# Kernel optimization log

Hardware: AMD Instinct MI355X
Metric: run time of the kernel (lower is better)

## Reference

```python
import jax, jax.numpy as jnp
import numpy as np

D_MODEL = 1024
HEADS = 16
D_K = D_MODEL // HEADS


def setup_inputs() -> dict:
    key = jax.random.key(0)
    ks = jax.random.split(key, 12)
    B, S = 2, 2048
    s = 1.0 / np.sqrt(D_MODEL)
    return {
        "queries": jax.random.normal(ks[0], (B, S, D_MODEL), jnp.float32),
        "keys": jax.random.normal(ks[1], (B, S, D_MODEL), jnp.float32),
        "values": jax.random.normal(ks[2], (B, S, D_MODEL), jnp.float32),
        "Wq": jax.random.normal(ks[3], (D_MODEL, D_MODEL), jnp.float32) * s,
        "bq": jnp.zeros((D_MODEL,), jnp.float32),
        "Wk": jax.random.normal(ks[4], (D_MODEL, D_MODEL), jnp.float32) * s,
        "bk": jnp.zeros((D_MODEL,), jnp.float32),
        "Wv": jax.random.normal(ks[5], (D_MODEL, D_MODEL), jnp.float32) * s,
        "bv": jnp.zeros((D_MODEL,), jnp.float32),
        "Wo": jax.random.normal(ks[6], (D_MODEL, D_MODEL), jnp.float32) * s,
        "bo": jnp.zeros((D_MODEL,), jnp.float32),
        "gamma": jnp.ones((D_MODEL,), jnp.float32),
        "beta": jnp.zeros((D_MODEL,), jnp.float32),
    }


def reference(queries, keys, values, Wq, bq, Wk, bk, Wv, bv, Wo, bo, gamma, beta):
    B, Nq, D = queries.shape
    Nk = keys.shape[1]
    # projections (torch Linear: x @ W.T + b), split into heads
    q = (queries @ Wq.T + bq).reshape(B, Nq, HEADS, D_K).transpose(0, 2, 1, 3)  # [B,H,Nq,dk]
    k = (keys @ Wk.T + bk).reshape(B, Nk, HEADS, D_K).transpose(0, 2, 1, 3)     # [B,H,Nk,dk]
    v = (values @ Wv.T + bv).reshape(B, Nk, HEADS, D_K).transpose(0, 2, 1, 3)   # [B,H,Nk,dv]
    att = jnp.einsum("bhqd,bhkd->bhqk", q, k) / np.sqrt(D_K).astype(np.float32)
    att = jax.nn.softmax(att, axis=-1)
    out = jnp.einsum("bhqk,bhkd->bhqd", att, v)
    out = out.transpose(0, 2, 1, 3).reshape(B, Nq, HEADS * D_K)
    out = out @ Wo.T + bo
    # dropout_prob=0 -> identity; residual shortcut then LayerNorm
    out = queries + out
    mean = jnp.mean(out, axis=-1, keepdims=True)
    var = jnp.var(out, axis=-1, keepdims=True)
    out = (out - mean) / jnp.sqrt(var + 1e-5) * gamma + beta
    return out
```

## Files before the change

kernel.cpp:

```cpp
#include <hip/hip_runtime.h>

#define S_LEN 2048
#define BATCH 2
#define DM 1024
#define NH 16
#define DK 64
#define M_ROWS 4096

typedef __bf16 bf16x8 __attribute__((ext_vector_type(8)));
typedef float f32x4 __attribute__((ext_vector_type(4)));
typedef unsigned int u32;
typedef unsigned short u16;

__device__ __forceinline__ float bf2f(u16 u) {
    union { u32 i; float f; } v;
    v.i = ((u32)u) << 16;
    return v.f;
}

__device__ __forceinline__ u16 rne16(float f) {
    u32 i = __builtin_bit_cast(u32, f);
    return (u16)((i + 0x7fffu + ((i >> 16) & 1u)) >> 16);
}

__device__ __forceinline__ u32 pk2(float x, float y) {
    u32 a = __builtin_bit_cast(u32, x) + 0x8000u;
    u32 b = __builtin_bit_cast(u32, y) + 0x8000u;
    return (a >> 16) | (b & 0xffff0000u);
}

__device__ __forceinline__ void async16(const void* g, void* l) {
    __builtin_amdgcn_global_load_lds(
        (const __attribute__((address_space(1))) u32*)((unsigned long long)g),
        (__attribute__((address_space(3))) u32*)((u32)(unsigned long long)l),
        16, 0, 0);
}

__global__ __launch_bounds__(256) void cvt_all(
    const float* __restrict__ q, const float* __restrict__ k,
    const float* __restrict__ v, const float* __restrict__ wq,
    const float* __restrict__ wk, const float* __restrict__ wv,
    const float* __restrict__ wo,
    u16* q16, u16* k16, u16* v16, u16* wq16, u16* wk16, u16* wv16, u16* wo16)
{
    const int b = blockIdx.x;
    const float* src; u16* dst; long off;
    if (b < 2048)      { src = q;  dst = q16;  off = (long)b * 2048; }
    else if (b < 4096) { src = k;  dst = k16;  off = (long)(b - 2048) * 2048; }
    else if (b < 6144) { src = v;  dst = v16;  off = (long)(b - 4096) * 2048; }
    else if (b < 6656) { src = wq; dst = wq16; off = (long)(b - 6144) * 2048; }
    else if (b < 7168) { src = wk; dst = wk16; off = (long)(b - 6656) * 2048; }
    else if (b < 7680) { src = wv; dst = wv16; off = (long)(b - 7168) * 2048; }
    else               { src = wo; dst = wo16; off = (long)(b - 7680) * 2048; }
    const long i = off + (long)threadIdx.x * 8;
    const float4 a = *(const float4*)(src + i);
    const float4 c = *(const float4*)(src + i + 4);
    uint4 r;
    r.x = pk2(a.x, a.y); r.y = pk2(a.z, a.w);
    r.z = pk2(c.x, c.y); r.w = pk2(c.z, c.w);
    *(uint4*)(dst + i) = r;
}

__global__ __launch_bounds__(256) void gemm64(
    const u16* __restrict__ A0, const u16* __restrict__ W0,
    const float* __restrict__ bias0, u16* __restrict__ C0, float sc0, int md0,
    const u16* __restrict__ A1, const u16* __restrict__ W1,
    const float* __restrict__ bias1, u16* __restrict__ C1, float sc1, int md1)
{
    __shared__ u16 sA[128 * 32];
    __shared__ u16 sB[64 * 32];

    const u16* A = blockIdx.z ? A1 : A0;
    const u16* W = blockIdx.z ? W1 : W0;
    const float* bias = blockIdx.z ? bias1 : bias0;
    u16* C = blockIdx.z ? C1 : C0;
    const float scale = blockIdx.z ? sc1 : sc0;
    const int mode = blockIdx.z ? md1 : md0;

    const int t    = threadIdx.x;
    const int lane = t & 63;
    const int wave = t >> 6;
    const int quad = lane >> 4;
    const int lr   = lane & 15;
    const int wm   = wave * 32;
    const int m0   = blockIdx.y * 128;
    const int n0   = blockIdx.x * 64;

    f32x4 acc[2][4];
#pragma unroll
    for (int i = 0; i < 2; i++)
#pragma unroll
        for (int j = 0; j < 4; j++) acc[i][j] = (f32x4){0.f, 0.f, 0.f, 0.f};

    const int la1 = t + 256;
    const int ra0 = t >> 2,   ca0 = (t & 3)   ^ (ra0 & 3);
    const int ra1 = la1 >> 2, ca1 = (la1 & 3) ^ (ra1 & 3);
    const int rb  = t >> 2,   cb  = (t & 3)   ^ (rb & 3);
    const u16* gA0 = A + (long)(m0 + ra0) * 1024 + ca0 * 8;
    const u16* gA1 = A + (long)(m0 + ra1) * 1024 + ca1 * 8;
    const u16* gW  = W + (long)(n0 + rb) * 1024 + cb * 8;

    const int sw = quad ^ (lr & 3);

    for (int k0 = 0; k0 < 1024; k0 += 32) {
        __syncthreads();
        async16(gA0 + k0, &sA[t * 8]);
        async16(gA1 + k0, &sA[la1 * 8]);
        async16(gW + k0, &sB[t * 8]);
        __syncthreads();

        bf16x8 aF[2], bF[4];
#pragma unroll
        for (int i = 0; i < 2; i++)
            aF[i] = *(const bf16x8*)&sA[((wm + i * 16 + lr) * 4 + sw) * 8];
#pragma unroll
        for (int j = 0; j < 4; j++)
            bF[j] = *(const bf16x8*)&sB[((j * 16 + lr) * 4 + sw) * 8];
#pragma unroll
        for (int i = 0; i < 2; i++)
#pragma unroll
            for (int j = 0; j < 4; j++)
                acc[i][j] = __builtin_amdgcn_mfma_f32_16x16x32_bf16(
                    aF[i], bF[j], acc[i][j], 0, 0, 0);
    }

#pragma unroll
    for (int j = 0; j < 4; j++) {
        const int gn = n0 + j * 16 + lr;
        const float bvv = bias[gn];
#pragma unroll
        for (int i = 0; i < 2; i++) {
            const int gmb = m0 + wm + i * 16 + quad * 4;
#pragma unroll
            for (int r = 0; r < 4; r++) {
                const int gm = gmb + r;
                const float val = (acc[i][j][r] + bvv) * scale;
                long idx;
                if (mode == 1) {
                    idx = (long)(gm >> 11) * (NH * S_LEN * DK)
                        + (long)(gn >> 6) * (S_LEN * DK)
                        + (long)(gm & (S_LEN - 1)) * DK + (gn & (DK - 1));
                } else if (mode == 2) {
                    idx = ((long)(gm >> 11) * NH + (gn >> 6)) * (DK * S_LEN)
                        + (long)(gn & (DK - 1)) * S_LEN + (gm & (S_LEN - 1));
                } else {
                    idx = (long)gm * 1024 + gn;
                }
                C[idx] = rne16(val);
            }
        }
    }
}

__global__ __launch_bounds__(256, 2) void attn_flash(
    const u16* __restrict__ Q,
    const u16* __restrict__ K,
    const u16* __restrict__ Vt,
    u16* __restrict__ Out)
{
    __shared__ u16 sK[2][8192];
    __shared__ u16 sP[128 * 80];

    const int t    = threadIdx.x;
    const int lane = t & 63;
    const int wave = t >> 6;
    const int quad = lane >> 4;
    const int lr   = lane & 15;
    const int q0   = blockIdx.x * 128;
    const int bh   = blockIdx.y;

    const long baseQK = (long)bh * S_LEN * DK;
    const long baseV  = (long)bh * DK * S_LEN;

#pragma unroll
    for (int i = 0; i < 4; i++) {
        const int l = t + i * 256;
        const int row = l >> 3, c8 = l & 7;
        *(uint4*)&sP[row * 72 + c8 * 8] =
            *(const uint4*)(Q + baseQK + (long)(q0 + row) * DK + c8 * 8);
    }

    const u16* gK[4];
#pragma unroll
    for (int i = 0; i < 4; i++) {
        const int l = t + i * 256;
        const int h = l >> 9, rem = l & 511;
        const int row = rem >> 2, c = (rem & 3) ^ (row & 3);
        gK[i] = K + baseQK + row * DK + h * 32 + c * 8;
    }
#pragma unroll
    for (int i = 0; i < 4; i++)
        async16(gK[i], &sK[0][(t + i * 256) * 8]);
    __syncthreads();

    bf16x8 qf[2][2];
#pragma unroll
    for (int s = 0; s < 2; s++)
#pragma unroll
        for (int h = 0; h < 2; h++)
            qf[s][h] = *(const bf16x8*)&sP[(s * 64 + wave * 16 + lr) * 72 + h * 32 + quad * 8];

    f32x4 oacc[2][4];
#pragma unroll
    for (int s = 0; s < 2; s++)
#pragma unroll
        for (int nj = 0; nj < 4; nj++) oacc[s][nj] = (f32x4){0.f, 0.f, 0.f, 0.f};
    float m_run[2] = {-1e30f, -1e30f}, l_run[2] = {0.f, 0.f};

    const int sw = quad ^ (lr & 3);

    for (int kb = 0; kb < S_LEN / 128; kb++) {
        const int buf = kb & 1, nb = buf ^ 1;
        __syncthreads();

        uint4 bvr[16];
#pragma unroll
        for (int nj = 0; nj < 4; nj++)
#pragma unroll
            for (int kk = 0; kk < 4; kk++)
                bvr[nj * 4 + kk] = *(const uint4*)(Vt + baseV
                    + (long)(nj * 16 + lr) * S_LEN + kb * 128 + kk * 32 + quad * 8);

        if (kb + 1 < S_LEN / 128) {
#pragma unroll
            for (int i = 0; i < 4; i++)
                async16(gK[i] + (long)(kb + 1) * 128 * DK, &sK[nb][(t + i * 256) * 8]);
        }

        f32x4 sacc[8][2];
#pragma unroll
        for (int mi = 0; mi < 8; mi++) {
            const bf16x8 a0 = *(const bf16x8*)&sK[buf][(((mi * 16 + lr) * 4) + sw) * 8];
            const bf16x8 a1 = *(const bf16x8*)&sK[buf][((512 + (mi * 16 + lr) * 4) + sw) * 8];
            const f32x4 z = (f32x4){0.f, 0.f, 0.f, 0.f};
            sacc[mi][0] = __builtin_amdgcn_mfma_f32_16x16x32_bf16(
                a1, qf[0][1],
                __builtin_amdgcn_mfma_f32_16x16x32_bf16(a0, qf[0][0], z, 0, 0, 0), 0, 0, 0);
            sacc[mi][1] = __builtin_amdgcn_mfma_f32_16x16x32_bf16(
                a1, qf[1][1],
                __builtin_amdgcn_mfma_f32_16x16x32_bf16(a0, qf[1][0], z, 0, 0, 0), 0, 0, 0);
        }

#pragma unroll
        for (int s = 0; s < 2; s++) {
            float mloc = -1e30f;
#pragma unroll
            for (int mi = 0; mi < 8; mi++)
#pragma unroll
                for (int r = 0; r < 4; r++) mloc = fmaxf(mloc, sacc[mi][s][r]);
            mloc = fmaxf(mloc, __shfl_xor(mloc, 16, 64));
            mloc = fmaxf(mloc, __shfl_xor(mloc, 32, 64));
            const float m_new = fmaxf(m_run[s], mloc);
            const float alpha = __builtin_amdgcn_exp2f(m_run[s] - m_new);
            m_run[s] = m_new;

            float psum = 0.f;
#pragma unroll
            for (int mi = 0; mi < 8; mi++)
#pragma unroll
                for (int r = 0; r < 4; r++) {
                    const float p = __builtin_amdgcn_exp2f(sacc[mi][s][r] - m_new);
                    sacc[mi][s][r] = p;
                    psum += p;
                }
            psum += __shfl_xor(psum, 16, 64);
            psum += __shfl_xor(psum, 32, 64);
            l_run[s] = l_run[s] * alpha + psum;

            float ar[4];
#pragma unroll
            for (int r = 0; r < 4; r++) ar[r] = __shfl(alpha, quad * 4 + r, 64);
#pragma unroll
            for (int nj = 0; nj < 4; nj++)
#pragma unroll
                for (int r = 0; r < 4; r++) oacc[s][nj][r] *= ar[r];

            const int prow = s * 64 + wave * 16 + lr;
#pragma unroll
            for (int mi = 0; mi < 8; mi++) {
                uint2 w;
                w.x = pk2(sacc[mi][s][0], sacc[mi][s][1]);
                w.y = pk2(sacc[mi][s][2], sacc[mi][s][3]);
                *(uint2*)&sP[prow * 80 + mi * 16 + quad * 4] = w;
            }
#pragma unroll
            for (int kk = 0; kk < 4; kk++) {
                const bf16x8 pa = *(const bf16x8*)&sP[prow * 80 + kk * 32 + quad * 8];
#pragma unroll
                for (int nj = 0; nj < 4; nj++) {
                    const bf16x8 bb = *(const bf16x8*)&bvr[nj * 4 + kk];
                    oacc[s][nj] = __builtin_amdgcn_mfma_f32_16x16x32_bf16(
                        pa, bb, oacc[s][nj], 0, 0, 0);
                }
            }
        }
    }

    const int b = bh >> 4, h = bh & (NH - 1);
#pragma unroll
    for (int s = 0; s < 2; s++) {
        const float inv = 1.0f / l_run[s];
        float ivr[4];
#pragma unroll
        for (int r = 0; r < 4; r++) ivr[r] = __shfl(inv, quad * 4 + r, 64);
#pragma unroll
        for (int nj = 0; nj < 4; nj++)
#pragma unroll
            for (int r = 0; r < 4; r++) {
                const int qg = q0 + s * 64 + wave * 16 + quad * 4 + r;
                const long oi = ((long)(b * S_LEN + qg)) * DM + h * DK + nj * 16 + lr;
                Out[oi] = rne16(oacc[s][nj][r] * ivr[r]);
            }
    }
}

__global__ __launch_bounds__(256) void ln_res(
    const float* __restrict__ X,
    const u16* __restrict__ O,
    const float* __restrict__ gamma,
    const float* __restrict__ beta,
    float* __restrict__ Out)
{
    __shared__ float sR[8];
    const int row = blockIdx.x;
    const int t = threadIdx.x;
    const int lane = t & 63, wave = t >> 6;
    const long off = (long)row * DM + t * 4;

    const float4 x4 = *(const float4*)(X + off);
    const uint2  uo = *(const uint2*)(O + off);
    float x[4];
    x[0] = x4.x + bf2f((u16)(uo.x & 0xffffu));
    x[1] = x4.y + bf2f((u16)(uo.x >> 16));
    x[2] = x4.z + bf2f((u16)(uo.y & 0xffffu));
    x[3] = x4.w + bf2f((u16)(uo.y >> 16));

    float s  = x[0] + x[1] + x[2] + x[3];
    float ss = x[0] * x[0] + x[1] * x[1] + x[2] * x[2] + x[3] * x[3];
#pragma unroll
    for (int o2 = 32; o2 > 0; o2 >>= 1) {
        s  += __shfl_xor(s, o2, 64);
        ss += __shfl_xor(ss, o2, 64);
    }
    if (lane == 0) { sR[wave] = s; sR[4 + wave] = ss; }
    __syncthreads();
    if (t == 0) {
        sR[0] = sR[0] + sR[1] + sR[2] + sR[3];
        sR[4] = sR[4] + sR[5] + sR[6] + sR[7];
    }
    __syncthreads();
    const float mean = sR[0] * (1.0f / DM);
    const float var  = sR[4] * (1.0f / DM) - mean * mean;
    const float rstd = rsqrtf(var + 1e-5f);

    const float4 g4 = *(const float4*)(gamma + t * 4);
    const float4 b4 = *(const float4*)(beta + t * 4);
    float4 r;
    r.x = (x[0] - mean) * rstd * g4.x + b4.x;
    r.y = (x[1] - mean) * rstd * g4.y + b4.y;
    r.z = (x[2] - mean) * rstd * g4.z + b4.z;
    r.w = (x[3] - mean) * rstd * g4.w + b4.w;
    *(float4*)(Out + off) = r;
}

extern "C" void kernel_launch(void* const* d_in, const int* in_sizes, int n_in,
                              void* d_out, int out_size, void* d_ws, size_t ws_size,
                              hipStream_t stream)
{
    (void)in_sizes; (void)n_in; (void)out_size; (void)ws_size;
    const float* queries = (const float*)d_in[0];
    const float* keys    = (const float*)d_in[1];
    const float* values  = (const float*)d_in[2];
    const float* Wq = (const float*)d_in[3];
    const float* bq = (const float*)d_in[4];
    const float* Wk = (const float*)d_in[5];
    const float* bk = (const float*)d_in[6];
    const float* Wv = (const float*)d_in[7];
    const float* bv = (const float*)d_in[8];
    const float* Wo = (const float*)d_in[9];
    const float* bo = (const float*)d_in[10];
    const float* gamma = (const float*)d_in[11];
    const float* beta  = (const float*)d_in[12];

    char* ws = (char*)d_ws;
    const size_t MB = (size_t)1024 * 1024;
    u16* Q16  = (u16*)(ws);
    u16* K16  = (u16*)(ws + 8 * MB);
    u16* Wq16 = (u16*)(ws + 16 * MB);
    u16* Wk16 = (u16*)(ws + 18 * MB);
    u16* Wv16 = (u16*)(ws + 20 * MB);
    u16* Wo16 = (u16*)(ws + 22 * MB);
    u16* Kb   = (u16*)(ws + 24 * MB);
    u16* Ob   = Q16;
    u16* Vtb  = K16;
    u16* V16  = (u16*)d_out;
    u16* Qb   = (u16*)((char*)d_out + 8 * MB);
    u16* Ab   = (u16*)d_out;

    const float CS = 0.18033688011112042f;

    cvt_all<<<8192, 256, 0, stream>>>(queries, keys, values, Wq, Wk, Wv, Wo,
                                      Q16, K16, V16, Wq16, Wk16, Wv16, Wo16);
    gemm64<<<dim3(16, 32, 2), 256, 0, stream>>>(
        Q16, Wq16, bq, Qb, CS, 1,
        K16, Wk16, bk, Kb, 1.0f, 1);
    gemm64<<<dim3(16, 32, 1), 256, 0, stream>>>(
        V16, Wv16, bv, Vtb, 1.0f, 2,
        V16, Wv16, bv, Vtb, 1.0f, 2);
    attn_flash<<<dim3(S_LEN / 128, BATCH * NH), 256, 0, stream>>>(Qb, Kb, Vtb, Ab);
    gemm64<<<dim3(16, 32, 1), 256, 0, stream>>>(
        Ab, Wo16, bo, Ob, 1.0f, 3,
        Ab, Wo16, bo, Ob, 1.0f, 3);
    ln_res<<<M_ROWS, 256, 0, stream>>>(queries, Ob, gamma, beta, (float*)d_out);
}
```

Baseline: 277.6 us.

## Double-buffer projection GEMMs, widen tiles, merge QKV launch, stage stores through LDS

Replaces the single-buffered 128x64 GEMM with a templated kernel using 128-wide N tiles (BM of 128 or 64) and double-buffered shared memory. The next K-slice is prefetched while the current one is multiplied, which removes one barrier per iteration. The Q, K and V projections now run in one three-slice launch. Epilogues stage results through LDS so the head-split and transposed V layouts are written with coalesced 16-byte stores instead of scattered 2-byte stores. The trade-off is more shared memory per block and extra epilogue barriers.

Result: faster. 258.2 us (-7.0%).

```diff
diff --git a/kernel.cpp b/kernel.cpp
--- a/kernel.cpp
+++ b/kernel.cpp
@@ -61,92 +61,178 @@
     *(uint4*)(dst + i) = r;
 }
 
-__global__ __launch_bounds__(256) void gemm64(
+template <int BM>
+__global__ __launch_bounds__(256) void gemm_t(
     const u16* __restrict__ A0, const u16* __restrict__ W0,
-    const float* __restrict__ bias0, u16* __restrict__ C0, float sc0, int md0,
+    const float* __restrict__ bi0, u16* __restrict__ C0, float s0, int md0,
     const u16* __restrict__ A1, const u16* __restrict__ W1,
-    const float* __restrict__ bias1, u16* __restrict__ C1, float sc1, int md1)
+    const float* __restrict__ bi1, u16* __restrict__ C1, float s1, int md1,
+    const u16* __restrict__ A2, const u16* __restrict__ W2,
+    const float* __restrict__ bi2, u16* __restrict__ C2, float s2, int md2)
 {
-    __shared__ u16 sA[128 * 32];
-    __shared__ u16 sB[64 * 32];
-
-    const u16* A = blockIdx.z ? A1 : A0;
-    const u16* W = blockIdx.z ? W1 : W0;
-    const float* bias = blockIdx.z ? bias1 : bias0;
-    u16* C = blockIdx.z ? C1 : C0;
-    const float scale = blockIdx.z ? sc1 : sc0;
-    const int mode = blockIdx.z ? md1 : md0;
+    constexpr int IT = BM / 32;
+    constexpr int ASZ = BM * 32;
+    constexpr int BSZ = 128 * 32;
+    __shared__ u16 smem[2 * ASZ + 2 * BSZ];
+
+    const int z = blockIdx.z;
+    const u16* A = z == 0 ? A0 : (z == 1 ? A1 : A2);
+    const u16* W = z == 0 ? W0 : (z == 1 ? W1 : W2);
+    const float* bias = z == 0 ? bi0 : (z == 1 ? bi1 : bi2);
+    u16* C = z == 0 ? C0 : (z == 1 ? C1 : C2);
+    const float scale = z == 0 ? s0 : (z == 1 ? s1 : s2);
+    const int mode = z == 0 ? md0 : (z == 1 ? md1 : md2);
 
     const int t    = threadIdx.x;
     const int lane = t & 63;
     const int wave = t >> 6;
     const int quad = lane >> 4;
     const int lr   = lane & 15;
-    const int wm   = wave * 32;
-    const int m0   = blockIdx.y * 128;
-    const int n0   = blockIdx.x * 64;
-
-    f32x4 acc[2][4];
-#pragma unroll
-    for (int i = 0; i < 2; i++)
+    const int wm   = (wave >> 1) * (BM / 2);
+    const int wn   = (wave & 1) * 64;
+    const int m0   = blockIdx.y * BM;
+    const int n0   = blockIdx.x * 128;
+
+    f32x4 acc[IT][4];
+#pragma unroll
+    for (int i = 0; i < IT; i++)
 #pragma unroll
         for (int j = 0; j < 4; j++) acc[i][j] = (f32x4){0.f, 0.f, 0.f, 0.f};
 
-    const int la1 = t + 256;
-    const int ra0 = t >> 2,   ca0 = (t & 3)   ^ (ra0 & 3);
-    const int ra1 = la1 >> 2, ca1 = (la1 & 3) ^ (ra1 & 3);
-    const int rb  = t >> 2,   cb  = (t & 3)   ^ (rb & 3);
-    const u16* gA0 = A + (long)(m0 + ra0) * 1024 + ca0 * 8;
-    const u16* gA1 = A + (long)(m0 + ra1) * 1024 + ca1 * 8;
-    const u16* gW  = W + (long)(n0 + rb) * 1024 + cb * 8;
+    const u16 *gA0, *gA1 = nullptr, *gW0, *gW1;
+    {
+        int c = t, r = c >> 2, cc = (c & 3) ^ (r & 3);
+        gA0 = A + (long)(m0 + r) * 1024 + cc * 8;
+        if (BM == 128) {
+            c = t + 256; r = c >> 2; cc = (c & 3) ^ (r & 3);
+            gA1 = A + (long)(m0 + r) * 1024 + cc * 8;
+        }
+        c = t; r = c >> 2; cc = (c & 3) ^ (r & 3);
+        gW0 = W + (long)(n0 + r) * 1024 + cc * 8;
+        c = t + 256; r = c >> 2; cc = (c & 3) ^ (r & 3);
+        gW1 = W + (long)(n0 + r) * 1024 + cc * 8;
+    }
+
+    async16(gA0, smem + t * 8);
+    if constexpr (BM == 128) async16(gA1, smem + (t + 256) * 8);
+    async16(gW0, smem + 2 * ASZ + t * 8);
+    async16(gW1, smem + 2 * ASZ + (t + 256) * 8);
 
     const int sw = quad ^ (lr & 3);
 
-    for (int k0 = 0; k0 < 1024; k0 += 32) {
+    for (int kb = 0; kb < 32; kb++) {
         __syncthreads();
-        async16(gA0 + k0, &sA[t * 8]);
-        async16(gA1 + k0, &sA[la1 * 8]);
-        async16(gW + k0, &sB[t * 8]);
-        __syncthreads();
-
-        bf16x8 aF[2], bF[4];
-#pragma unroll
-        for (int i = 0; i < 2; i++)
-            aF[i] = *(const bf16x8*)&sA[((wm + i * 16 + lr) * 4 + sw) * 8];
+        if (kb < 31) {
+            const int k1 = (kb + 1) * 32;
+            u16* dA = smem + ((kb + 1) & 1) * ASZ;
+            u16* dB = smem + 2 * ASZ + ((kb + 1) & 1) * BSZ;
+            async16(gA0 + k1, dA + t * 8);
+            if constexpr (BM == 128) async16(gA1 + k1, dA + (t + 256) * 8);
+            async16(gW0 + k1, dB + t * 8);
+            async16(gW1 + k1, dB + (t + 256) * 8);
+        }
+        const u16* sa = smem + (kb & 1) * ASZ;
+        const u16* sb = smem + 2 * ASZ + (kb & 1) * BSZ;
+        bf16x8 aF[IT], bF[4];
+#pragma unroll
+        for (int i = 0; i < IT; i++)
+            aF[i] = *(const bf16x8*)&sa[((wm + i * 16 + lr) * 4 + sw) * 8];
 #pragma unroll
         for (int j = 0; j < 4; j++)
-            bF[j] = *(const bf16x8*)&sB[((j * 16 + lr) * 4 + sw) * 8];
-#pragma unroll
-        for (int i = 0; i < 2; i++)
+            bF[j] = *(const bf16x8*)&sb[((wn + j * 16 + lr) * 4 + sw) * 8];
+#pragma unroll
+        for (int i = 0; i < IT; i++)
 #pragma unroll
             for (int j = 0; j < 4; j++)
                 acc[i][j] = __builtin_amdgcn_mfma_f32_16x16x32_bf16(
                     aF[i], bF[j], acc[i][j], 0, 0, 0);
     }
 
-#pragma unroll
-    for (int j = 0; j < 4; j++) {
-        const int gn = n0 + j * 16 + lr;
-        const float bvv = bias[gn];
-#pragma unroll
-        for (int i = 0; i < 2; i++) {
-            const int gmb = m0 + wm + i * 16 + quad * 4;
-#pragma unroll
-            for (int r = 0; r < 4; r++) {
-                const int gm = gmb + r;
-                const float val = (acc[i][j][r] + bvv) * scale;
-                long idx;
-                if (mode == 1) {
-                    idx = (long)(gm >> 11) * (NH * S_LEN * DK)
-                        + (long)(gn >> 6) * (S_LEN * DK)
-                        + (long)(gm & (S_LEN - 1)) * DK + (gn & (DK - 1));
-                } else if (mode == 2) {
-                    idx = ((long)(gm >> 11) * NH + (gn >> 6)) * (DK * S_LEN)
-                        + (long)(gn & (DK - 1)) * S_LEN + (gm & (S_LEN - 1));
-                } else {
-                    idx = (long)gm * 1024 + gn;
+    u16* sO = smem;
+    const int b_ = m0 >> 11;
+
+    if constexpr (BM == 64) {
+        __syncthreads();
+#pragma unroll
+        for (int i = 0; i < IT; i++)
+#pragma unroll
+            for (int j = 0; j < 4; j++) {
+                const float bvv = bias[n0 + wn + j * 16 + lr];
+#pragma unroll
+                for (int r = 0; r < 4; r++) {
+                    const int gmL = wm + i * 16 + quad * 4 + r;
+                    sO[gmL * 136 + wn + j * 16 + lr] =
+                        rne16((acc[i][j][r] + bvv) * scale);
                 }
-                C[idx] = rne16(val);
+            }
+        __syncthreads();
+#pragma unroll
+        for (int i = 0; i < 4; i++) {
+            const int c = t + i * 256;
+            const int row = c >> 4, c8 = c & 15;
+            *(uint4*)(C + (long)(m0 + row) * 1024 + n0 + c8 * 8) =
+                *(const uint4*)&sO[row * 136 + c8 * 8];
+        }
+    } else if (mode == 1) {
+#pragma unroll
+        for (int pass = 0; pass < 2; pass++) {
+            __syncthreads();
+            if ((wave >> 1) == pass) {
+#pragma unroll
+                for (int i = 0; i < IT; i++)
+#pragma unroll
+                    for (int j = 0; j < 4; j++) {
+                        const float bvv = bias[n0 + wn + j * 16 + lr];
+#pragma unroll
+                        for (int r = 0; r < 4; r++) {
+                            const int gmL = i * 16 + quad * 4 + r;
+                            sO[gmL * 136 + wn + j * 16 + lr] =
+                                rne16((acc[i][j][r] + bvv) * scale);
+                        }
+                    }
+            }
+            __syncthreads();
+#pragma unroll
+            for (int i = 0; i < 4; i++) {
+                const int c = t + i * 256;
+                const int row = c >> 4, c8 = c & 15;
+                const int gm = m0 + pass * 64 + row;
+                const int gn = n0 + c8 * 8;
+                const long idx = (((long)b_ * NH + (gn >> 6)) * S_LEN
+                                  + (gm & (S_LEN - 1))) * DK + (gn & 63);
+                *(uint4*)(C + idx) = *(const uint4*)&sO[row * 136 + c8 * 8];
+            }
+        }
+    } else {
+#pragma unroll
+        for (int pass = 0; pass < 2; pass++) {
+            __syncthreads();
+            if ((wave >> 1) == pass) {
+#pragma unroll
+                for (int i = 0; i < IT; i++)
+#pragma unroll
+                    for (int j = 0; j < 4; j++) {
+                        const float bvv = bias[n0 + wn + j * 16 + lr];
+                        const u16 v0 = rne16((acc[i][j][0] + bvv) * scale);
+                        const u16 v1 = rne16((acc[i][j][1] + bvv) * scale);
+                        const u16 v2 = rne16((acc[i][j][2] + bvv) * scale);
+                        const u16 v3 = rne16((acc[i][j][3] + bvv) * scale);
+                        uint2 w;
+                        w.x = (u32)v0 | ((u32)v1 << 16);
+                        w.y = (u32)v2 | ((u32)v3 << 16);
+                        *(uint2*)&sO[(wn + j * 16 + lr) * 72 + i * 16 + quad * 4] = w;
+                    }
+            }
+            __syncthreads();
+#pragma unroll
+            for (int i = 0; i < 4; i++) {
+                const int c = t + i * 256;
+                const int row = c >> 3, c8 = c & 7;
+                const int gn = n0 + row;
+                const int s = m0 + pass * 64 + c8 * 8;
+                const long idx = (((long)b_ * NH + (gn >> 6)) * DK
+                                  + (gn & 63)) * S_LEN + (s & (S_LEN - 1));
+                *(uint4*)(C + idx) = *(const uint4*)&sO[row * 72 + c8 * 8];
             }
         }
     }
@@ -401,14 +487,13 @@
 
     cvt_all<<<8192, 256, 0, stream>>>(queries, keys, values, Wq, Wk, Wv, Wo,
                                       Q16, K16, V16, Wq16, Wk16, Wv16, Wo16);
-    gemm64<<<dim3(16, 32, 2), 256, 0, stream>>>(
+    gemm_t<128><<<dim3(8, 32, 3), 256, 0, stream>>>(
         Q16, Wq16, bq, Qb, CS, 1,
-        K16, Wk16, bk, Kb, 1.0f, 1);
-    gemm64<<<dim3(16, 32, 1), 256, 0, stream>>>(
-        V16, Wv16, bv, Vtb, 1.0f, 2,
+        K16, Wk16, bk, Kb, 1.0f, 1,
         V16, Wv16, bv, Vtb, 1.0f, 2);
     attn_flash<<<dim3(S_LEN / 128, BATCH * NH), 256, 0, stream>>>(Qb, Kb, Vtb, Ab);
-    gemm64<<<dim3(16, 32, 1), 256, 0, stream>>>(
+    gemm_t<64><<<dim3(8, 64, 1), 256, 0, stream>>>(
+        Ab, Wo16, bo, Ob, 1.0f, 3,
         Ab, Wo16, bo, Ob, 1.0f, 3,
         Ab, Wo16, bo, Ob, 1.0f, 3);
     ln_res<<<M_ROWS, 256, 0, stream>>>(queries, Ob, gamma, beta, (float*)d_out);
```
